# Optimization experiments

Hardware: AMD Instinct MI355X
Metric: run time of the kernel (lower is better)

Reference implementation:

```python
import jax, jax.numpy as jnp
import numpy as np

N_NODES = 50000
N_EDGES = 800000
N_REL = 3
N_GRAPHS = 500
EMB = 128
IN_DIM = EMB * 3
HID = 256
N_CLASS = 10
N_SHAPE, N_COLOR, MAX_POS = 8, 8, 128


def rgcn_layer(h, src, dst, etype, W, root, b):
    """PyG RGCNConv with default aggr='mean':
    out[v] = sum_r mean_{(j->v) in E_r} h[j] @ W[r] + h[v] @ root + b
    Aggregate raw features per (dst, relation) bucket, then apply relation matmuls.
    """
    N, R = h.shape[0], W.shape[0]
    seg = dst * R + etype  # combined (node, relation) segment id
    sums = jax.ops.segment_sum(h[src], seg, num_segments=N * R)          # (N*R, d)
    cnt = jax.ops.segment_sum(jnp.ones(seg.shape, h.dtype), seg, num_segments=N * R)
    mean = (sums / jnp.maximum(cnt, 1.0)[:, None]).reshape(N, R, -1)     # (N, R, d)
    return jnp.einsum('nrd,rdh->nh', mean, W) + h @ root + b


def setup_inputs() -> dict:
    key = jax.random.key(0)
    ks = jax.random.split(key, 20)
    f32 = jnp.float32
    inp = {
        's': jax.random.randint(ks[0], (N_NODES,), 0, N_SHAPE),
        'c': jax.random.randint(ks[1], (N_NODES,), 0, N_COLOR),
        'p': jax.random.randint(ks[2], (N_NODES,), 0, MAX_POS),
        'edge_index': jax.random.randint(ks[3], (2, N_EDGES), 0, N_NODES),
        'edge_type': jax.random.randint(ks[4], (N_EDGES,), 0, N_REL),
        'batch': jnp.sort(jax.random.randint(ks[5], (N_NODES,), 0, N_GRAPHS)),
        'shape_emb': jax.random.normal(ks[6], (N_SHAPE, EMB), f32),
        'color_emb': jax.random.normal(ks[7], (N_COLOR, EMB), f32),
        'pos_emb': jax.random.normal(ks[8], (MAX_POS, EMB), f32),
        'W1': jax.random.normal(ks[9], (N_REL, IN_DIM, HID), f32) / np.sqrt(IN_DIM),
        'root1': jax.random.normal(ks[10], (IN_DIM, HID), f32) / np.sqrt(IN_DIM),
        'b1': jnp.zeros((HID,), f32),
        'W2': jax.random.normal(ks[11], (N_REL, HID, HID), f32) / np.sqrt(HID),
        'root2': jax.random.normal(ks[12], (HID, HID), f32) / np.sqrt(HID),
        'b2': jnp.zeros((HID,), f32),
        'lin_w': jax.random.normal(ks[13], (HID, N_CLASS), f32) / np.sqrt(HID),
        'lin_b': jnp.zeros((N_CLASS,), f32),
    }
    return inp


def reference(s, c, p, edge_index, edge_type, batch,
              shape_emb, color_emb, pos_emb,
              W1, root1, b1, W2, root2, b2, lin_w, lin_b):
    src, dst = edge_index[0], edge_index[1]
    h = jnp.concatenate([shape_emb[s], color_emb[c], pos_emb[p]], axis=-1)  # (N, 3*emb)
    h = jax.nn.relu(rgcn_layer(h, src, dst, edge_type, W1, root1, b1))
    h = jax.nn.relu(rgcn_layer(h, src, dst, edge_type, W2, root2, b2))
    # global_mean_pool over graphs
    gsum = jax.ops.segment_sum(h, batch, num_segments=N_GRAPHS)
    gcnt = jax.ops.segment_sum(jnp.ones((h.shape[0],), h.dtype), batch, num_segments=N_GRAPHS)
    pooled = gsum / jnp.maximum(gcnt, 1.0)[:, None]
    return pooled @ lin_w + lin_b
```

## Files before the change

### kernel.cpp

```cpp
#include <hip/hip_runtime.h>
#include <hip/hip_bf16.h>

#define NN 50000
#define NE 800000
#define NR 3
#define NG 500
#define NB (NN * NR)
#define NCLS 10
#define NCMB 8192
#define CHUNK 2048
#define NBLK ((NB + CHUNK - 1) / CHUNK)

#define P1_COMBO   196
#define P1_ZCNT    586
#define P1_ZPOOL   502
#define P1_TAB     576
#define P1_WF      1024
#define P1_TOTAL   (P1_COMBO + P1_ZCNT + P1_ZPOOL + P1_TAB + P1_WF)
#define P2_CNT     3125
#define P2_TB      768
#define P2_TOTAL   (P2_CNT + P2_TB)

typedef __hip_bfloat16 bf16;
typedef __attribute__((ext_vector_type(8))) short short8;
typedef __attribute__((ext_vector_type(4))) float floatx4;

static __device__ __forceinline__ float b2f(bf16 x) { return __bfloat162float(x); }
static __device__ __forceinline__ bf16  f2b(float x) { return __float2bfloat16(x); }
static __device__ __forceinline__ float bs2f(short x) {
    return __bfloat162float(*reinterpret_cast<const bf16*>(&x));
}
static __device__ __forceinline__ short f2bs(float x) {
    bf16 b = __float2bfloat16(x);
    return *reinterpret_cast<const short*>(&b);
}

__global__ __launch_bounds__(256) void prep1(const int* __restrict__ s,
                                             const int* __restrict__ c,
                                             const int* __restrict__ p,
                                             const float* __restrict__ se,
                                             const float* __restrict__ ce,
                                             const float* __restrict__ pe,
                                             const float* __restrict__ W1,
                                             const float* __restrict__ root1,
                                             const float* __restrict__ W2,
                                             const float* __restrict__ root2,
                                             int* __restrict__ combo,
                                             unsigned* __restrict__ cnt,
                                             unsigned* __restrict__ poolz,
                                             float* __restrict__ tab,
                                             bf16* __restrict__ Wf) {
    int b = blockIdx.x, t = threadIdx.x;
    if (b < P1_COMBO) {
        int n = b * 256 + t;
        if (n < NN) combo[n] = (s[n] << 10) | (c[n] << 7) | p[n];
        return;
    }
    b -= P1_COMBO;
    if (b < P1_ZCNT) {
        int i = b * 256 + t;
        if (i < NB) cnt[i] = 0u;
        return;
    }
    b -= P1_ZCNT;
    if (b < P1_ZPOOL) {
        int i = b * 256 + t;
        if (i < NG * 256 + NG) poolz[i] = 0u;
        return;
    }
    b -= P1_ZPOOL;
    if (b < P1_TAB) {
        int r = b / 144, row = b % 144;
        const float* A; int segk;
        if (row < 8)       { A = se + row * 128;        segk = 0; }
        else if (row < 16) { A = ce + (row - 8) * 128;  segk = 128; }
        else               { A = pe + (row - 16) * 128; segk = 256; }
        const float* W = (r < 3) ? (W1 + (size_t)r * 384 * 256) : root1;
        float acc = 0.f;
        for (int k = 0; k < 128; ++k)
            acc += A[k] * W[(size_t)(segk + k) * 256 + t];
        tab[((size_t)r * 144 + row) * 256 + t] = acc;
        return;
    }
    b -= P1_TAB;
    {
        int idx = b * 256 + t;
        int j     = idx & 7;
        int lane  = (idx >> 3) & 63;
        int ni    = (idx >> 9) & 3;
        int chunk = (idx >> 11) & 31;
        int colblk = idx >> 16;
        int col = colblk * 64 + ni * 16 + (lane & 15);
        int k   = chunk * 32 + (lane >> 4) * 8 + j;
        float v = (k < 768) ? W2[((size_t)(k >> 8) * 256 + (k & 255)) * 256 + col]
                            : root2[(size_t)(k - 768) * 256 + col];
        Wf[idx] = f2b(v);
    }
}

__global__ __launch_bounds__(256) void prep2(const int* __restrict__ ei,
                                             const int* __restrict__ et,
                                             int* __restrict__ cnt,
                                             const float* __restrict__ tab,
                                             const float* __restrict__ b1,
                                             bf16* __restrict__ tb2) {
    int b = blockIdx.x, t = threadIdx.x;
    if (b < P2_CNT) {
        int e = b * 256 + t;
        if (e < NE) atomicAdd(&cnt[ei[NE + e] * NR + et[e]], 1);
        return;
    }
    b -= P2_CNT;
    if (b < 256) {
        int r = b >> 6, sc = b & 63, si = sc >> 3, ci = sc & 7;
        float v = tab[((size_t)r * 144 + si) * 256 + t]
                + tab[((size_t)r * 144 + 8 + ci) * 256 + t];
        if (r == 3) v += b1[t];
        tb2[(size_t)b * 256 + t] = f2b(v);
    } else {
        int bb = b - 256;
        int r = bb >> 7, pi = bb & 127;
        tb2[(size_t)(256 + bb) * 256 + t] =
            f2b(tab[((size_t)r * 144 + 16 + pi) * 256 + t]);
    }
}

__global__ __launch_bounds__(256) void scan_block_sums(const int* __restrict__ cnt,
                                                       int* __restrict__ bsum) {
    __shared__ int sm[256];
    int b = blockIdx.x, t = threadIdx.x;
    int base = b * CHUNK + t * 8, s = 0;
#pragma unroll
    for (int j = 0; j < 8; ++j) { int i = base + j; if (i < NB) s += cnt[i]; }
    sm[t] = s; __syncthreads();
    for (int st = 128; st; st >>= 1) { if (t < st) sm[t] += sm[t + st]; __syncthreads(); }
    if (!t) bsum[b] = sm[0];
}

__global__ __launch_bounds__(256) void scan_write(const int* __restrict__ cnt,
                                                  const int* __restrict__ bsum,
                                                  int* __restrict__ off,
                                                  int* __restrict__ cursor) {
    int b = blockIdx.x, t = threadIdx.x;
    int bbase = 0;
    for (int i = 0; i < b; ++i) bbase += bsum[i];
    if (b == 0 && t == 0) {
        int tot = 0;
        for (int i = 0; i < NBLK; ++i) tot += bsum[i];
        off[NB] = tot;
    }
    int base = b * CHUNK + t * 8;
    int v[8], ts = 0;
#pragma unroll
    for (int j = 0; j < 8; ++j) { int i = base + j; v[j] = (i < NB) ? cnt[i] : 0; ts += v[j]; }
    int lane = t & 63, wv = t >> 6;
    int incl = ts;
    for (int d = 1; d < 64; d <<= 1) {
        int o = __shfl_up(incl, d, 64);
        if (lane >= d) incl += o;
    }
    __shared__ int wsum[4];
    if (lane == 63) wsum[wv] = incl;
    __syncthreads();
    int wbase = 0;
    for (int w = 0; w < wv; ++w) wbase += wsum[w];
    int run = bbase + wbase + incl - ts;
#pragma unroll
    for (int j = 0; j < 8; ++j) {
        int i = base + j;
        if (i < NB) { off[i] = run; cursor[i] = run; }
        run += v[j];
    }
}

__global__ __launch_bounds__(256) void scatter_edges(const int* __restrict__ ei,
                                                     const int* __restrict__ et,
                                                     const int* __restrict__ combo,
                                                     int* __restrict__ cursor,
                                                     unsigned* __restrict__ esc) {
    int e = blockIdx.x * 256 + threadIdx.x;
    if (e >= NE) return;
    int b = ei[NE + e] * NR + et[e];
    int pos = atomicAdd(&cursor[b], 1);
    int s = ei[e];
    esc[pos] = ((unsigned)s << 13) | (unsigned)combo[s];
}

__global__ __launch_bounds__(256) void l1_fused(const int* __restrict__ off,
                                                const unsigned* __restrict__ esc,
                                                const int* __restrict__ combo,
                                                const bf16* __restrict__ tb2,
                                                bf16* __restrict__ h1) {
    int wave = threadIdx.x >> 6, lane = threadIdx.x & 63;
    int dst = blockIdx.x * 4 + wave;
    if (dst >= NN) return;
    int half = lane >> 5, li8 = (lane & 31) * 8;
    int b0 = dst * NR;
    int o0 = off[b0], o1 = off[b0 + 1], o2 = off[b0 + 2], o3 = off[b0 + 3];
    float inv0 = (o1 > o0) ? 1.f / (float)(o1 - o0) : 0.f;
    float inv1 = (o2 > o1) ? 1.f / (float)(o2 - o1) : 0.f;
    float inv2 = (o3 > o2) ? 1.f / (float)(o3 - o2) : 0.f;
    float rootf[8] = {};
    if (half == 0) {
        int cmbD = combo[dst];
        short8 rsc = *(const short8*)(tb2 + (size_t)(192 + (cmbD >> 7)) * 256 + li8);
        short8 rp  = *(const short8*)(tb2 + (size_t)(640 + (cmbD & 127)) * 256 + li8);
#pragma unroll
        for (int i = 0; i < 8; ++i) rootf[i] = bs2f(rsc[i]) + bs2f(rp[i]);
    }
    float s[8] = {};
    int j = o0;
    for (; j + 8 <= o3; j += 8) {
        int k0 = j + half, k1 = j + 2 + half, k2 = j + 4 + half, k3 = j + 6 + half;
        unsigned e0 = esc[k0], e1 = esc[k1], e2 = esc[k2], e3 = esc[k3];
        int r0 = (k0 >= o1) + (k0 >= o2);
        int r1 = (k1 >= o1) + (k1 >= o2);
        int r2 = (k2 >= o1) + (k2 >= o2);
        int r3 = (k3 >= o1) + (k3 >= o2);
        short8 sc0 = *(const short8*)(tb2 + (size_t)(r0 * 64 + ((e0 & 8191) >> 7)) * 256 + li8);
        short8 sp0 = *(const short8*)(tb2 + (size_t)(256 + r0 * 128 + (e0 & 127)) * 256 + li8);
        short8 sc1 = *(const short8*)(tb2 + (size_t)(r1 * 64 + ((e1 & 8191) >> 7)) * 256 + li8);
        short8 sp1 = *(const short8*)(tb2 + (size_t)(256 + r1 * 128 + (e1 & 127)) * 256 + li8);
        short8 sc2 = *(const short8*)(tb2 + (size_t)(r2 * 64 + ((e2 & 8191) >> 7)) * 256 + li8);
        short8 sp2 = *(const short8*)(tb2 + (size_t)(256 + r2 * 128 + (e2 & 127)) * 256 + li8);
        short8 sc3 = *(const short8*)(tb2 + (size_t)(r3 * 64 + ((e3 & 8191) >> 7)) * 256 + li8);
        short8 sp3 = *(const short8*)(tb2 + (size_t)(256 + r3 * 128 + (e3 & 127)) * 256 + li8);
        float w0 = (k0 >= o2) ? inv2 : ((k0 >= o1) ? inv1 : inv0);
        float w1 = (k1 >= o2) ? inv2 : ((k1 >= o1) ? inv1 : inv0);
        float w2 = (k2 >= o2) ? inv2 : ((k2 >= o1) ? inv1 : inv0);
        float w3 = (k3 >= o2) ? inv2 : ((k3 >= o1) ? inv1 : inv0);
#pragma unroll
        for (int i = 0; i < 8; ++i)
            s[i] += (bs2f(sc0[i]) + bs2f(sp0[i])) * w0
                  + (bs2f(sc1[i]) + bs2f(sp1[i])) * w1
                  + (bs2f(sc2[i]) + bs2f(sp2[i])) * w2
                  + (bs2f(sc3[i]) + bs2f(sp3[i])) * w3;
    }
    for (; j + 2 <= o3; j += 2) {
        int k0 = j + half;
        unsigned e0 = esc[k0];
        int r0 = (k0 >= o1) + (k0 >= o2);
        short8 sc0 = *(const short8*)(tb2 + (size_t)(r0 * 64 + ((e0 & 8191) >> 7)) * 256 + li8);
        short8 sp0 = *(const short8*)(tb2 + (size_t)(256 + r0 * 128 + (e0 & 127)) * 256 + li8);
        float w0 = (k0 >= o2) ? inv2 : ((k0 >= o1) ? inv1 : inv0);
#pragma unroll
        for (int i = 0; i < 8; ++i) s[i] += (bs2f(sc0[i]) + bs2f(sp0[i])) * w0;
    }
    if (j < o3 && half == 0) {
        int k0 = j;
        unsigned e0 = esc[k0];
        int r0 = (k0 >= o1) + (k0 >= o2);
        short8 sc0 = *(const short8*)(tb2 + (size_t)(r0 * 64 + ((e0 & 8191) >> 7)) * 256 + li8);
        short8 sp0 = *(const short8*)(tb2 + (size_t)(256 + r0 * 128 + (e0 & 127)) * 256 + li8);
        float w0 = (k0 >= o2) ? inv2 : ((k0 >= o1) ? inv1 : inv0);
#pragma unroll
        for (int i = 0; i < 8; ++i) s[i] += (bs2f(sc0[i]) + bs2f(sp0[i])) * w0;
    }
    short8 o;
#pragma unroll
    for (int i = 0; i < 8; ++i) {
        float tot = s[i] + __shfl_xor(s[i], 32);
        o[i] = f2bs(fmaxf(rootf[i] + tot, 0.f));
    }
    if (half == 0)
        *(short8*)(h1 + (size_t)dst * 256 + li8) = o;
}

__global__ __launch_bounds__(256) void agg_all(const int* __restrict__ off,
                                               const unsigned* __restrict__ esc,
                                               const bf16* __restrict__ h1,
                                               bf16* __restrict__ hagg) {
    int wave = threadIdx.x >> 6, lane = threadIdx.x & 63;
    int dst = blockIdx.x * 4 + wave;
    if (dst >= NN) return;
    int half = lane >> 5, li8 = (lane & 31) * 8;
    int o0 = off[dst * NR],     o1 = off[dst * NR + 1],
        o2 = off[dst * NR + 2], o3 = off[dst * NR + 3];
    float s0[8] = {}, s1[8] = {}, s2[8] = {};
    int n = max((o1 - o0 + 1) >> 1, max((o2 - o1 + 1) >> 1, (o3 - o2 + 1) >> 1));
    for (int k = 0; k < n; k += 2) {
#pragma unroll
        for (int kk = 0; kk < 2; ++kk) {
            int i0 = o0 + 2 * (k + kk) + half;
            int i1 = o1 + 2 * (k + kk) + half;
            int i2 = o2 + 2 * (k + kk) + half;
            bool g0 = i0 < o1, g1 = i1 < o2, g2 = i2 < o3;
            unsigned e0 = esc[g0 ? i0 : 0];
            unsigned e1 = esc[g1 ? i1 : 0];
            unsigned e2 = esc[g2 ? i2 : 0];
            short8 v0 = *(const short8*)(h1 + (size_t)(g0 ? (e0 >> 13) : 0) * 256 + li8);
            short8 v1 = *(const short8*)(h1 + (size_t)(g1 ? (e1 >> 13) : 0) * 256 + li8);
            short8 v2 = *(const short8*)(h1 + (size_t)(g2 ? (e2 >> 13) : 0) * 256 + li8);
            float m0 = g0 ? 1.f : 0.f, m1 = g1 ? 1.f : 0.f, m2 = g2 ? 1.f : 0.f;
#pragma unroll
            for (int i = 0; i < 8; ++i) {
                s0[i] += bs2f(v0[i]) * m0;
                s1[i] += bs2f(v1[i]) * m1;
                s2[i] += bs2f(v2[i]) * m2;
            }
        }
    }
    float inv0 = (o1 > o0) ? 1.f / (float)(o1 - o0) : 0.f;
    float inv1 = (o2 > o1) ? 1.f / (float)(o2 - o1) : 0.f;
    float inv2 = (o3 > o2) ? 1.f / (float)(o3 - o2) : 0.f;
    short8 w0, w1, w2;
#pragma unroll
    for (int i = 0; i < 8; ++i) {
        float t0 = s0[i] + __shfl_xor(s0[i], 32);
        float t1 = s1[i] + __shfl_xor(s1[i], 32);
        float t2 = s2[i] + __shfl_xor(s2[i], 32);
        w0[i] = f2bs(t0 * inv0);
        w1[i] = f2bs(t1 * inv1);
        w2[i] = f2bs(t2 * inv2);
    }
    if (half == 0) {
        bf16* hd = hagg + (size_t)dst * 768 + li8;
        *(short8*)(hd)       = w0;
        *(short8*)(hd + 256) = w1;
        *(short8*)(hd + 512) = w2;
    }
}

__global__ __launch_bounds__(256) void gemm_cat(const bf16* __restrict__ hagg,
                                                const bf16* __restrict__ h1,
                                                const bf16* __restrict__ Wf,
                                                const float* __restrict__ bias,
                                                const int* __restrict__ batch,
                                                float* __restrict__ pool,
                                                float* __restrict__ gcnt) {
    __shared__ short lds[4][2][32 * 40];
    const int t = threadIdx.x;
    const int wave = t >> 6, lane = t & 63;
    const int quad = lane >> 4, l16 = lane & 15;
    const int row0 = blockIdx.x * 32;
    const int colblk = wave;
    const int rsub = lane >> 2;
    const int ksub = (lane & 3) * 8;
    short* A0 = lds[wave][0];
    short* A1 = lds[wave][1];

    const int r0 = min(row0 + rsub, NN - 1);
    const int r1 = min(row0 + 16 + rsub, NN - 1);
    const bf16* gA0 = hagg + (size_t)r0 * 768 + ksub;
    const bf16* gA1 = hagg + (size_t)r1 * 768 + ksub;
    const bf16* gH0 = h1 + (size_t)r0 * 256 + ksub;
    const bf16* gH1 = h1 + (size_t)r1 * 256 + ksub;
    const short8* bbase = (const short8*)Wf + (size_t)colblk * 32 * 4 * 64 + lane;

    auto loadA2 = [&](int k0, short8& a0, short8& a1) {
        if (k0 < 768) { a0 = *(const short8*)(gA0 + k0); a1 = *(const short8*)(gA1 + k0); }
        else          { a0 = *(const short8*)(gH0 + k0 - 768); a1 = *(const short8*)(gH1 + k0 - 768); }
    };
    auto loadB = [&](int chunk, short8* bf4) {
        const short8* bp = bbase + (size_t)chunk * 4 * 64;
#pragma unroll
        for (int ni = 0; ni < 4; ++ni) bf4[ni] = bp[ni * 64];
    };

    floatx4 acc[2][4] = {};
    short8 aE0, aE1, bE[4];
    short8 aO0, aO1, bO[4];
    loadA2(0, aE0, aE1);  loadB(0, bE);
    loadA2(32, aO0, aO1); loadB(1, bO);

#pragma unroll
    for (int i = 0; i < 32; i += 2) {
        *(short8*)&A0[rsub * 40 + ksub] = aE0;
        *(short8*)&A0[(16 + rsub) * 40 + ksub] = aE1;
        {
            short8 af0 = *(const short8*)&A0[l16 * 40 + quad * 8];
            short8 af1 = *(const short8*)&A0[(16 + l16) * 40 + quad * 8];
#pragma unroll
            for (int ni = 0; ni < 4; ++ni) {
                acc[0][ni] = __builtin_amdgcn_mfma_f32_16x16x32_bf16(af0, bE[ni], acc[0][ni], 0, 0, 0);
                acc[1][ni] = __builtin_amdgcn_mfma_f32_16x16x32_bf16(af1, bE[ni], acc[1][ni], 0, 0, 0);
            }
        }
        if (i + 2 < 32) { loadA2((i + 2) * 32, aE0, aE1); loadB(i + 2, bE); }
        *(short8*)&A1[rsub * 40 + ksub] = aO0;
        *(short8*)&A1[(16 + rsub) * 40 + ksub] = aO1;
        {
            short8 af0 = *(const short8*)&A1[l16 * 40 + quad * 8];
            short8 af1 = *(const short8*)&A1[(16 + l16) * 40 + quad * 8];
#pragma unroll
            for (int ni = 0; ni < 4; ++ni) {
                acc[0][ni] = __builtin_amdgcn_mfma_f32_16x16x32_bf16(af0, bO[ni], acc[0][ni], 0, 0, 0);
                acc[1][ni] = __builtin_amdgcn_mfma_f32_16x16x32_bf16(af1, bO[ni], acc[1][ni], 0, 0, 0);
            }
        }
        if (i + 3 < 32) { loadA2((i + 3) * 32, aO0, aO1); loadB(i + 3, bO); }
    }

    __syncthreads();
    short* st = &lds[0][0][0];
#pragma unroll
    for (int mi = 0; mi < 2; ++mi) {
#pragma unroll
        for (int ni = 0; ni < 4; ++ni) {
            int n = colblk * 64 + ni * 16 + l16;
            float bn = bias[n];
#pragma unroll
            for (int ii = 0; ii < 4; ++ii) {
                int lrow = mi * 16 + quad * 4 + ii;
                float v = (row0 + lrow < NN) ? fmaxf(acc[mi][ni][ii] + bn, 0.f) : 0.f;
                st[lrow * 260 + n] = f2bs(v);
            }
        }
    }
    __syncthreads();
    int nrows = NN - row0; if (nrows > 32) nrows = 32;
    int curg = batch[row0];
    float a = 0.f, cntf = 0.f;
    for (int rr = 0; rr < nrows; ++rr) {
        int g = batch[row0 + rr];
        if (g != curg) {
            atomicAdd(&pool[(size_t)curg * 256 + t], a);
            if (t == 0) atomicAdd(&gcnt[curg], cntf);
            a = 0.f; cntf = 0.f; curg = g;
        }
        a += bs2f(st[rr * 260 + t]);
        cntf += 1.f;
    }
    atomicAdd(&pool[(size_t)curg * 256 + t], a);
    if (t == 0) atomicAdd(&gcnt[curg], cntf);
}

__global__ __launch_bounds__(256) void final_head(const float* __restrict__ pool,
                                                  const float* __restrict__ gcnt,
                                                  const float* __restrict__ lin_w,
                                                  const float* __restrict__ lin_b,
                                                  float* __restrict__ out) {
    __shared__ float sm[256];
    int g = blockIdx.x, t = threadIdx.x;
    float inv = 1.0f / fmaxf(gcnt[g], 1.0f);
    sm[t] = pool[(size_t)g * 256 + t] * inv;
    __syncthreads();
    if (t < NCLS) {
        float s = lin_b[t];
        for (int d = 0; d < 256; ++d) s += sm[d] * lin_w[d * NCLS + t];
        out[g * NCLS + t] = s;
    }
}

extern "C" void kernel_launch(void* const* d_in, const int* in_sizes, int n_in,
                              void* d_out, int out_size, void* d_ws, size_t ws_size,
                              hipStream_t stream) {
    const int*   s_idx = (const int*)d_in[0];
    const int*   c_idx = (const int*)d_in[1];
    const int*   p_idx = (const int*)d_in[2];
    const int*   ei    = (const int*)d_in[3];
    const int*   et    = (const int*)d_in[4];
    const int*   batch = (const int*)d_in[5];
    const float* se    = (const float*)d_in[6];
    const float* ce    = (const float*)d_in[7];
    const float* pe    = (const float*)d_in[8];
    const float* W1    = (const float*)d_in[9];
    const float* root1 = (const float*)d_in[10];
    const float* b1    = (const float*)d_in[11];
    const float* W2    = (const float*)d_in[12];
    const float* root2 = (const float*)d_in[13];
    const float* b2    = (const float*)d_in[14];
    const float* lin_w = (const float*)d_in[15];
    const float* lin_b = (const float*)d_in[16];
    float* out = (float*)d_out;

    char* w = (char*)d_ws;
    size_t o = 0;
    auto alloc = [&](size_t bytes) -> void* {
        o = (o + 15) & ~(size_t)15;
        void* ptr = w + o;
        o += bytes;
        return ptr;
    };
    bf16*     hagg   = (bf16*)    alloc((size_t)NN * 768 * 2);
    bf16*     h1     = (bf16*)    alloc((size_t)NN * 256 * 2);
    bf16*     tb2    = (bf16*)    alloc((size_t)768 * 256 * 2);
    int*      combo  = (int*)     alloc((size_t)NN * 4);
    unsigned* esc    = (unsigned*)alloc((size_t)NE * 4);
    int*      cnt    = (int*)     alloc((size_t)NB * 4);
    int*      off    = (int*)     alloc((size_t)(NB + 1) * 4);
    int*      cursor = (int*)     alloc((size_t)NB * 4);
    int*      bsum   = (int*)     alloc((size_t)NBLK * 4);
    float*    tab    = (float*)   alloc((size_t)4 * 144 * 256 * 4);
    bf16*     Wf     = (bf16*)    alloc((size_t)256 * 1024 * 2);
    float*    pool   = (float*)   alloc((size_t)NG * 256 * 4);
    float*    gcnt   = (float*)   alloc((size_t)NG * 4);
    (void)ws_size;

    prep1<<<P1_TOTAL, 256, 0, stream>>>(s_idx, c_idx, p_idx, se, ce, pe,
                                        W1, root1, W2, root2,
                                        combo, (unsigned*)cnt, (unsigned*)pool, tab, Wf);
    prep2<<<P2_TOTAL, 256, 0, stream>>>(ei, et, cnt, tab, b1, tb2);
    scan_block_sums<<<NBLK, 256, 0, stream>>>(cnt, bsum);
    scan_write<<<NBLK, 256, 0, stream>>>(cnt, bsum, off, cursor);
    scatter_edges<<<(NE + 255) / 256, 256, 0, stream>>>(ei, et, combo, cursor, esc);
    l1_fused<<<(NN + 3) / 4, 256, 0, stream>>>(off, esc, combo, tb2, h1);
    agg_all<<<(NN + 3) / 4, 256, 0, stream>>>(off, esc, h1, hagg);
    gemm_cat<<<(NN + 31) / 32, 256, 0, stream>>>(hagg, h1, Wf, b2, batch, pool, gcnt);
    final_head<<<NG, 256, 0, stream>>>(pool, gcnt, lin_w, lin_b, out);
}
```

Before: 377.2 us.

## Map full wave across feature row in gather kernels, drop half-wave edge split

Both gather kernels (l1_fused and agg_all) now have all 64 lanes cover the 256-wide feature row with 4-element loads, instead of two half-waves each handling alternate edges with 8-element loads and combining them by shuffle at the end. Edge loops are restructured into masked 8-wide (l1) and 4-wide (agg) batches so more gathers are in flight, and segment offsets are made wave-uniform via readfirstlane. The goal is to remove the cross-half reduction and tail handling and raise memory-level parallelism. The costs are narrower per-lane loads, and masked padding iterations that still issue loads for out-of-range slots.

```diff
diff --git a/kernel.cpp b/kernel.cpp
--- a/kernel.cpp
+++ b/kernel.cpp
@@ -23,6 +23,7 @@
 
 typedef __hip_bfloat16 bf16;
 typedef __attribute__((ext_vector_type(8))) short short8;
+typedef __attribute__((ext_vector_type(4))) short shortx4;
 typedef __attribute__((ext_vector_type(4))) float floatx4;
 
 static __device__ __forceinline__ float b2f(bf16 x) { return __bfloat162float(x); }
@@ -33,6 +34,9 @@
 static __device__ __forceinline__ short f2bs(float x) {
     bf16 b = __float2bfloat16(x);
     return *reinterpret_cast<const short*>(&b);
+}
+static __device__ __forceinline__ int rfl(int x) {
+    return __builtin_amdgcn_readfirstlane(x);
 }
 
 __global__ __launch_bounds__(256) void prep1(const int* __restrict__ s,
@@ -186,114 +190,80 @@
     esc[pos] = ((unsigned)s << 13) | (unsigned)combo[s];
 }
 
-__global__ __launch_bounds__(256) void l1_fused(const int* __restrict__ off,
-                                                const unsigned* __restrict__ esc,
-                                                const int* __restrict__ combo,
-                                                const bf16* __restrict__ tb2,
-                                                bf16* __restrict__ h1) {
+__global__ __launch_bounds__(256, 4) void l1_fused(const int* __restrict__ off,
+                                                   const unsigned* __restrict__ esc,
+                                                   const int* __restrict__ combo,
+                                                   const bf16* __restrict__ tb2,
+                                                   bf16* __restrict__ h1) {
     int wave = threadIdx.x >> 6, lane = threadIdx.x & 63;
     int dst = blockIdx.x * 4 + wave;
     if (dst >= NN) return;
-    int half = lane >> 5, li8 = (lane & 31) * 8;
+    int l4 = lane * 4;
     int b0 = dst * NR;
-    int o0 = off[b0], o1 = off[b0 + 1], o2 = off[b0 + 2], o3 = off[b0 + 3];
+    int o0 = rfl(off[b0]),     o1 = rfl(off[b0 + 1]),
+        o2 = rfl(off[b0 + 2]), o3 = rfl(off[b0 + 3]);
     float inv0 = (o1 > o0) ? 1.f / (float)(o1 - o0) : 0.f;
     float inv1 = (o2 > o1) ? 1.f / (float)(o2 - o1) : 0.f;
     float inv2 = (o3 > o2) ? 1.f / (float)(o3 - o2) : 0.f;
-    float rootf[8] = {};
-    if (half == 0) {
-        int cmbD = combo[dst];
-        short8 rsc = *(const short8*)(tb2 + (size_t)(192 + (cmbD >> 7)) * 256 + li8);
-        short8 rp  = *(const short8*)(tb2 + (size_t)(640 + (cmbD & 127)) * 256 + li8);
-#pragma unroll
-        for (int i = 0; i < 8; ++i) rootf[i] = bs2f(rsc[i]) + bs2f(rp[i]);
-    }
-    float s[8] = {};
-    int j = o0;
-    for (; j + 8 <= o3; j += 8) {
-        int k0 = j + half, k1 = j + 2 + half, k2 = j + 4 + half, k3 = j + 6 + half;
-        unsigned e0 = esc[k0], e1 = esc[k1], e2 = esc[k2], e3 = esc[k3];
-        int r0 = (k0 >= o1) + (k0 >= o2);
-        int r1 = (k1 >= o1) + (k1 >= o2);
-        int r2 = (k2 >= o1) + (k2 >= o2);
-        int r3 = (k3 >= o1) + (k3 >= o2);
-        short8 sc0 = *(const short8*)(tb2 + (size_t)(r0 * 64 + ((e0 & 8191) >> 7)) * 256 + li8);
-        short8 sp0 = *(const short8*)(tb2 + (size_t)(256 + r0 * 128 + (e0 & 127)) * 256 + li8);
-        short8 sc1 = *(const short8*)(tb2 + (size_t)(r1 * 64 + ((e1 & 8191) >> 7)) * 256 + li8);
-        short8 sp1 = *(const short8*)(tb2 + (size_t)(256 + r1 * 128 + (e1 & 127)) * 256 + li8);
-        short8 sc2 = *(const short8*)(tb2 + (size_t)(r2 * 64 + ((e2 & 8191) >> 7)) * 256 + li8);
-        short8 sp2 = *(const short8*)(tb2 + (size_t)(256 + r2 * 128 + (e2 & 127)) * 256 + li8);
-        short8 sc3 = *(const short8*)(tb2 + (size_t)(r3 * 64 + ((e3 & 8191) >> 7)) * 256 + li8);
-        short8 sp3 = *(const short8*)(tb2 + (size_t)(256 + r3 * 128 + (e3 & 127)) * 256 + li8);
-        float w0 = (k0 >= o2) ? inv2 : ((k0 >= o1) ? inv1 : inv0);
-        float w1 = (k1 >= o2) ? inv2 : ((k1 >= o1) ? inv1 : inv0);
-        float w2 = (k2 >= o2) ? inv2 : ((k2 >= o1) ? inv1 : inv0);
-        float w3 = (k3 >= o2) ? inv2 : ((k3 >= o1) ? inv1 : inv0);
-#pragma unroll
-        for (int i = 0; i < 8; ++i)
-            s[i] += (bs2f(sc0[i]) + bs2f(sp0[i])) * w0
-                  + (bs2f(sc1[i]) + bs2f(sp1[i])) * w1
-                  + (bs2f(sc2[i]) + bs2f(sp2[i])) * w2
-                  + (bs2f(sc3[i]) + bs2f(sp3[i])) * w3;
-    }
-    for (; j + 2 <= o3; j += 2) {
-        int k0 = j + half;
-        unsigned e0 = esc[k0];
-        int r0 = (k0 >= o1) + (k0 >= o2);
-        short8 sc0 = *(const short8*)(tb2 + (size_t)(r0 * 64 + ((e0 & 8191) >> 7)) * 256 + li8);
-        short8 sp0 = *(const short8*)(tb2 + (size_t)(256 + r0 * 128 + (e0 & 127)) * 256 + li8);
-        float w0 = (k0 >= o2) ? inv2 : ((k0 >= o1) ? inv1 : inv0);
-#pragma unroll
-        for (int i = 0; i < 8; ++i) s[i] += (bs2f(sc0[i]) + bs2f(sp0[i])) * w0;
-    }
-    if (j < o3 && half == 0) {
-        int k0 = j;
-        unsigned e0 = esc[k0];
-        int r0 = (k0 >= o1) + (k0 >= o2);
-        short8 sc0 = *(const short8*)(tb2 + (size_t)(r0 * 64 + ((e0 & 8191) >> 7)) * 256 + li8);
-        short8 sp0 = *(const short8*)(tb2 + (size_t)(256 + r0 * 128 + (e0 & 127)) * 256 + li8);
-        float w0 = (k0 >= o2) ? inv2 : ((k0 >= o1) ? inv1 : inv0);
-#pragma unroll
-        for (int i = 0; i < 8; ++i) s[i] += (bs2f(sc0[i]) + bs2f(sp0[i])) * w0;
-    }
-    short8 o;
-#pragma unroll
-    for (int i = 0; i < 8; ++i) {
-        float tot = s[i] + __shfl_xor(s[i], 32);
-        o[i] = f2bs(fmaxf(rootf[i] + tot, 0.f));
-    }
-    if (half == 0)
-        *(short8*)(h1 + (size_t)dst * 256 + li8) = o;
-}
-
-__global__ __launch_bounds__(256) void agg_all(const int* __restrict__ off,
-                                               const unsigned* __restrict__ esc,
-                                               const bf16* __restrict__ h1,
-                                               bf16* __restrict__ hagg) {
+    int cmbD = rfl(combo[dst]);
+    shortx4 rsc = *(const shortx4*)(tb2 + (size_t)(192 + (cmbD >> 7)) * 256 + l4);
+    shortx4 rp  = *(const shortx4*)(tb2 + (size_t)(640 + (cmbD & 127)) * 256 + l4);
+    float s[4];
+#pragma unroll
+    for (int i = 0; i < 4; ++i) s[i] = bs2f(rsc[i]) + bs2f(rp[i]);
+
+    for (int jb = o0; jb < o3; jb += 8) {
+        shortx4 sc[8], sp[8]; float w[8];
+#pragma unroll
+        for (int q = 0; q < 8; ++q) {
+            int k = jb + q;
+            bool g = k < o3;
+            int kk = g ? k : o0;
+            unsigned e = esc[kk];
+            int r = (kk >= o1) + (kk >= o2);
+            w[q] = g ? ((k >= o2) ? inv2 : ((k >= o1) ? inv1 : inv0)) : 0.f;
+            sc[q] = *(const shortx4*)(tb2 + (size_t)(r * 64 + ((e & 8191) >> 7)) * 256 + l4);
+            sp[q] = *(const shortx4*)(tb2 + (size_t)(256 + r * 128 + (e & 127)) * 256 + l4);
+        }
+#pragma unroll
+        for (int q = 0; q < 8; ++q)
+#pragma unroll
+            for (int i = 0; i < 4; ++i)
+                s[i] += (bs2f(sc[q][i]) + bs2f(sp[q][i])) * w[q];
+    }
+    shortx4 o;
+#pragma unroll
+    for (int i = 0; i < 4; ++i) o[i] = f2bs(fmaxf(s[i], 0.f));
+    *(shortx4*)(h1 + (size_t)dst * 256 + l4) = o;
+}
+
+__global__ __launch_bounds__(256, 4) void agg_all(const int* __restrict__ off,
+                                                  const unsigned* __restrict__ esc,
+                                                  const bf16* __restrict__ h1,
+                                                  bf16* __restrict__ hagg) {
     int wave = threadIdx.x >> 6, lane = threadIdx.x & 63;
     int dst = blockIdx.x * 4 + wave;
     if (dst >= NN) return;
-    int half = lane >> 5, li8 = (lane & 31) * 8;
-    int o0 = off[dst * NR],     o1 = off[dst * NR + 1],
-        o2 = off[dst * NR + 2], o3 = off[dst * NR + 3];
-    float s0[8] = {}, s1[8] = {}, s2[8] = {};
-    int n = max((o1 - o0 + 1) >> 1, max((o2 - o1 + 1) >> 1, (o3 - o2 + 1) >> 1));
-    for (int k = 0; k < n; k += 2) {
-#pragma unroll
-        for (int kk = 0; kk < 2; ++kk) {
-            int i0 = o0 + 2 * (k + kk) + half;
-            int i1 = o1 + 2 * (k + kk) + half;
-            int i2 = o2 + 2 * (k + kk) + half;
+    int l4 = lane * 4;
+    int b0 = dst * NR;
+    int o0 = rfl(off[b0]),     o1 = rfl(off[b0 + 1]),
+        o2 = rfl(off[b0 + 2]), o3 = rfl(off[b0 + 3]);
+    float s0[4] = {}, s1[4] = {}, s2[4] = {};
+    int n = max(o1 - o0, max(o2 - o1, o3 - o2));
+    for (int k = 0; k < n; k += 4) {
+#pragma unroll
+        for (int kk = 0; kk < 4; ++kk) {
+            int i0 = o0 + k + kk, i1 = o1 + k + kk, i2 = o2 + k + kk;
             bool g0 = i0 < o1, g1 = i1 < o2, g2 = i2 < o3;
             unsigned e0 = esc[g0 ? i0 : 0];
             unsigned e1 = esc[g1 ? i1 : 0];
             unsigned e2 = esc[g2 ? i2 : 0];
-            short8 v0 = *(const short8*)(h1 + (size_t)(g0 ? (e0 >> 13) : 0) * 256 + li8);
-            short8 v1 = *(const short8*)(h1 + (size_t)(g1 ? (e1 >> 13) : 0) * 256 + li8);
-            short8 v2 = *(const short8*)(h1 + (size_t)(g2 ? (e2 >> 13) : 0) * 256 + li8);
+            shortx4 v0 = *(const shortx4*)(h1 + (size_t)(g0 ? (e0 >> 13) : 0) * 256 + l4);
+            shortx4 v1 = *(const shortx4*)(h1 + (size_t)(g1 ? (e1 >> 13) : 0) * 256 + l4);
+            shortx4 v2 = *(const shortx4*)(h1 + (size_t)(g2 ? (e2 >> 13) : 0) * 256 + l4);
             float m0 = g0 ? 1.f : 0.f, m1 = g1 ? 1.f : 0.f, m2 = g2 ? 1.f : 0.f;
 #pragma unroll
-            for (int i = 0; i < 8; ++i) {
+            for (int i = 0; i < 4; ++i) {
                 s0[i] += bs2f(v0[i]) * m0;
                 s1[i] += bs2f(v1[i]) * m1;
                 s2[i] += bs2f(v2[i]) * m2;
@@ -303,22 +273,17 @@
     float inv0 = (o1 > o0) ? 1.f / (float)(o1 - o0) : 0.f;
     float inv1 = (o2 > o1) ? 1.f / (float)(o2 - o1) : 0.f;
     float inv2 = (o3 > o2) ? 1.f / (float)(o3 - o2) : 0.f;
-    short8 w0, w1, w2;
-#pragma unroll
-    for (int i = 0; i < 8; ++i) {
-        float t0 = s0[i] + __shfl_xor(s0[i], 32);
-        float t1 = s1[i] + __shfl_xor(s1[i], 32);
-        float t2 = s2[i] + __shfl_xor(s2[i], 32);
-        w0[i] = f2bs(t0 * inv0);
-        w1[i] = f2bs(t1 * inv1);
-        w2[i] = f2bs(t2 * inv2);
-    }
-    if (half == 0) {
-        bf16* hd = hagg + (size_t)dst * 768 + li8;
-        *(short8*)(hd)       = w0;
-        *(short8*)(hd + 256) = w1;
-        *(short8*)(hd + 512) = w2;
-    }
+    shortx4 w0, w1, w2;
+#pragma unroll
+    for (int i = 0; i < 4; ++i) {
+        w0[i] = f2bs(s0[i] * inv0);
+        w1[i] = f2bs(s1[i] * inv1);
+        w2[i] = f2bs(s2[i] * inv2);
+    }
+    bf16* hd = hagg + (size_t)dst * 768 + l4;
+    *(shortx4*)(hd)       = w0;
+    *(shortx4*)(hd + 256) = w1;
+    *(shortx4*)(hd + 512) = w2;
 }
 
 __global__ __launch_bounds__(256) void gemm_cat(const bf16* __restrict__ hagg,
```

After: 375.4 us. No clear change (-0.5%).
